# Optimization experiments

Hardware: AMD Instinct MI355X
Metric: run time of the kernel (lower is better)

The kernel has to match this reference:

```python
import jax, jax.numpy as jnp
import numpy as np

EPS_W = 1e-8   # weight reciprocal eps (matches torch code)
EPS_BN = 1e-5  # torch BatchNorm1d default eps


def _cdist(a, b):
    # a: [B,N,3], b: [B,M,3] -> [B,N,M] euclidean distances
    sq = (jnp.sum(a * a, -1)[:, :, None] + jnp.sum(b * b, -1)[:, None, :]
          - 2.0 * jnp.einsum('bnd,bmd->bnm', a, b))
    return jnp.sqrt(jnp.maximum(sq, 0.0))


def _bn_relu(x, gamma, beta):
    # x: [B,C,N]; training-mode batch norm over (B,N)
    mean = jnp.mean(x, axis=(0, 2), keepdims=True)
    var = jnp.mean((x - mean) ** 2, axis=(0, 2), keepdims=True)
    y = (x - mean) * jax.lax.rsqrt(var + EPS_BN)
    y = y * gamma[None, :, None] + beta[None, :, None]
    return jax.nn.relu(y)


def setup_inputs() -> dict:
    key = jax.random.key(0)
    ks = jax.random.split(key, 8)
    B, Np, Ns = 16, 1024, 4096
    Cp, Cs, Co = 256, 128, 256
    return {
        'xyz_prev': jax.random.normal(ks[0], (B, Np, 3), jnp.float32),
        'xyz_skip': jax.random.normal(ks[1], (B, Ns, 3), jnp.float32),
        'points_prev': jax.random.normal(ks[2], (B, Cp, Np), jnp.float32),
        'points_skip': jax.random.normal(ks[3], (B, Cs, Ns), jnp.float32),
        'W1': jax.random.normal(ks[4], (Co, Cp + Cs), jnp.float32) * 0.05,
        'g1': jnp.ones((Co,), jnp.float32),
        'b1': jnp.zeros((Co,), jnp.float32),
        'W2': jax.random.normal(ks[5], (Co, Co), jnp.float32) * 0.05,
        'g2': jnp.ones((Co,), jnp.float32),
        'b2': jnp.zeros((Co,), jnp.float32),
    }


def reference(xyz_prev, xyz_skip, points_prev, points_skip, W1, g1, b1, W2, g2, b2):
    dist = _cdist(xyz_skip, xyz_prev)                       # [B,Ns,Np]
    neg, idx = jax.lax.top_k(-dist, 3)                      # 3 smallest dists
    dist_recip = 1.0 / (dist + EPS_W)
    # NOTE: normalization is over ALL N_prev points (faithful to source)
    weight = dist_recip / jnp.sum(dist_recip, axis=2, keepdims=True)
    w3 = jnp.take_along_axis(weight, idx, axis=2)           # [B,Ns,3]
    pp = jnp.swapaxes(points_prev, 1, 2)                    # [B,Np,Cp]
    g = jnp.take_along_axis(pp[:, None, :, :], idx[..., None], axis=2)  # [B,Ns,3,Cp]
    interp = jnp.einsum('bnk,bnkc->bcn', w3, g)             # [B,Cp,Ns]
    x = jnp.concatenate([interp, points_skip], axis=1)      # [B,Cp+Cs,Ns]
    x = _bn_relu(jnp.einsum('bcn,oc->bon', x, W1), g1, b1)
    x = _bn_relu(jnp.einsum('bcn,oc->bon', x, W2), g2, b2)
    return x
```

## Files before the change

### kernel.cpp

```cpp
#include <hip/hip_runtime.h>
#include <math.h>

constexpr int NB  = 16;
constexpr int NP  = 1024;
constexpr int NS  = 4096;
constexpr int CP  = 256;
constexpr int CS  = 128;
constexpr int CIN = 384;
constexpr int CO  = 256;

constexpr int NCHUNK = 8;
constexpr int CHPTS  = NP / NCHUNK;

typedef unsigned int uint;
typedef unsigned short ushort_t;
typedef __attribute__((ext_vector_type(8))) short short8;
typedef __attribute__((ext_vector_type(4))) float f32x4;

__device__ __forceinline__ ushort_t f2bf(float f) {
  uint u = __float_as_uint(f);
  uint r = (u + 0x7fffu + ((u >> 16) & 1u)) >> 16;
  return (ushort_t)r;
}
__device__ __forceinline__ float bf2f(ushort_t u) {
  return __uint_as_float(((uint)u) << 16);
}

__device__ __forceinline__ void gload16(const void* g, void* l) {
  __builtin_amdgcn_global_load_lds(
      (const __attribute__((address_space(1))) uint*)g,
      (__attribute__((address_space(3))) uint*)l, 16, 0, 0);
}

__global__ __launch_bounds__(256) void topk_chunk_kernel(
    const float* __restrict__ xyz_prev, const float* __restrict__ xyz_skip,
    float* __restrict__ pbuf) {
  __shared__ float px[CHPTS], py[CHPTS], pz[CHPTS];
  int ng = blockIdx.x;
  int q  = blockIdx.y;
  int b  = blockIdx.z;
  int tid = threadIdx.x;
  if (tid < CHPTS) {
    const float* xp = xyz_prev + ((size_t)b * NP + q * CHPTS + tid) * 3;
    px[tid] = xp[0]; py[tid] = xp[1]; pz[tid] = xp[2];
  }
  __syncthreads();
  int n = ng * 256 + tid;
  const float* xq = xyz_skip + ((size_t)b * NS + n) * 3;
  float qx = xq[0], qy = xq[1], qz = xq[2];
  float d0 = INFINITY, d1 = INFINITY, d2 = INFINITY;
  int i0 = -1, i1 = -1, i2 = -1;
  float rsum = 0.f;
  int pbase = q * CHPTS;

  #define TK_BODY(PX, PY, PZ, PI)                                        \
    {                                                                    \
      float dx = (PX) - qx, dy = (PY) - qy, dz = (PZ) - qz;              \
      float sq = fmaf(dz, dz, fmaf(dy, dy, fmaf(dx, dx, 1e-16f)));       \
      rsum += __builtin_amdgcn_rsqf(sq);                                 \
      bool c0 = sq < d0, c1 = sq < d1, c2 = sq < d2;                     \
      int pi = (PI);                                                     \
      d2 = c2 ? (c1 ? d1 : sq) : d2;                                     \
      i2 = c2 ? (c1 ? i1 : pi) : i2;                                     \
      d1 = c1 ? (c0 ? d0 : sq) : d1;                                     \
      i1 = c1 ? (c0 ? i0 : pi) : i1;                                     \
      d0 = c0 ? sq : d0;                                                 \
      i0 = c0 ? pi : i0;                                                 \
    }

  for (int p = 0; p < CHPTS; p += 4) {
    float4 X = *(const float4*)&px[p];
    float4 Y = *(const float4*)&py[p];
    float4 Z = *(const float4*)&pz[p];
    TK_BODY(X.x, Y.x, Z.x, pbase + p + 0);
    TK_BODY(X.y, Y.y, Z.y, pbase + p + 1);
    TK_BODY(X.z, Y.z, Z.z, pbase + p + 2);
    TK_BODY(X.w, Y.w, Z.w, pbase + p + 3);
  }
  #undef TK_BODY

  size_t P = ((size_t)(b * NCHUNK + q) * NS + n) * 8;
  float4 v0 = make_float4(d0, d1, d2, rsum);
  float4 v1;
  v1.x = __int_as_float(i0); v1.y = __int_as_float(i1);
  v1.z = __int_as_float(i2); v1.w = 0.f;
  *(float4*)(pbuf + P) = v0;
  *(float4*)(pbuf + P + 4) = v1;
}

__global__ __launch_bounds__(256) void topk_merge_kernel(
    const float* __restrict__ pbuf, float* __restrict__ w3,
    int* __restrict__ idx3) {
  int gid = blockIdx.x * 256 + threadIdx.x;
  int b = gid >> 12;
  int n = gid & (NS - 1);
  float d0 = INFINITY, d1 = INFINITY, d2 = INFINITY;
  int i0 = -1, i1 = -1, i2 = -1;
  float rsum = 0.f;
  for (int q = 0; q < NCHUNK; q++) {
    size_t P = ((size_t)(b * NCHUNK + q) * NS + n) * 8;
    float4 v0 = *(const float4*)(pbuf + P);
    float4 v1 = *(const float4*)(pbuf + P + 4);
    rsum += v0.w;
    float ds[3] = {v0.x, v0.y, v0.z};
    int   is[3] = {__float_as_int(v1.x), __float_as_int(v1.y),
                   __float_as_int(v1.z)};
    #pragma unroll
    for (int k = 0; k < 3; k++) {
      float sq = ds[k]; int pi = is[k];
      bool c0 = sq < d0, c1 = sq < d1, c2 = sq < d2;
      d2 = c2 ? (c1 ? d1 : sq) : d2;
      i2 = c2 ? (c1 ? i1 : pi) : i2;
      d1 = c1 ? (c0 ? d0 : sq) : d1;
      i1 = c1 ? (c0 ? i0 : pi) : i1;
      d0 = c0 ? sq : d0;
      i0 = c0 ? pi : i0;
    }
  }
  float inv = 1.0f / rsum;
  size_t base = (size_t)gid * 3;
  w3[base + 0] = __builtin_amdgcn_rsqf(d0) * inv;
  w3[base + 1] = __builtin_amdgcn_rsqf(d1) * inv;
  w3[base + 2] = __builtin_amdgcn_rsqf(d2) * inv;
  idx3[base + 0] = i0; idx3[base + 1] = i1; idx3[base + 2] = i2;
}

__global__ __launch_bounds__(256) void wcast_kernel(
    const float* __restrict__ W1, const float* __restrict__ W2,
    ushort_t* __restrict__ W1b, ushort_t* __restrict__ W2b) {
  int t = blockIdx.x * 256 + threadIdx.x;
  int n1 = CO * CIN / 4;
  if (t < n1) {
    float4 v = *(const float4*)(W1 + t * 4);
    ushort4 o; o.x = f2bf(v.x); o.y = f2bf(v.y); o.z = f2bf(v.z); o.w = f2bf(v.w);
    *(ushort4*)(W1b + t * 4) = o;
  } else {
    int u = t - n1;
    float4 v = *(const float4*)(W2 + u * 4);
    ushort4 o; o.x = f2bf(v.x); o.y = f2bf(v.y); o.z = f2bf(v.z); o.w = f2bf(v.w);
    *(ushort4*)(W2b + u * 4) = o;
  }
}

__global__ __launch_bounds__(256) void ppT_kernel(
    const float* __restrict__ pp, ushort_t* __restrict__ pptT) {
  __shared__ float tl[64][65];
  int p0 = blockIdx.x * 64, c0 = blockIdx.y * 64, b = blockIdx.z;
  int tid = threadIdx.x;
  const float* P = pp + (size_t)b * CP * NP;
  int pi4 = (tid & 15) * 4, ci = tid >> 4;
  #pragma unroll
  for (int r = 0; r < 4; r++) {
    int cc = ci + 16 * r;
    float4 v = *(const float4*)(P + (size_t)(c0 + cc) * NP + p0 + pi4);
    tl[cc][pi4] = v.x; tl[cc][pi4 + 1] = v.y; tl[cc][pi4 + 2] = v.z; tl[cc][pi4 + 3] = v.w;
  }
  __syncthreads();
  ushort_t* O = pptT + (size_t)b * NP * CP;
  int ci4 = (tid & 15) * 4, pi = tid >> 4;
  #pragma unroll
  for (int r = 0; r < 4; r++) {
    int pr = pi + 16 * r;
    ushort4 o;
    o.x = f2bf(tl[ci4 + 0][pr]); o.y = f2bf(tl[ci4 + 1][pr]);
    o.z = f2bf(tl[ci4 + 2][pr]); o.w = f2bf(tl[ci4 + 3][pr]);
    *(ushort4*)(O + (size_t)(p0 + pr) * CP + c0 + ci4) = o;
  }
}

__global__ __launch_bounds__(256) void skipT_kernel(
    const float* __restrict__ sk, ushort_t* __restrict__ x1) {
  __shared__ float tl[64][65];
  int n0 = blockIdx.x * 64, c0 = blockIdx.y * 64, b = blockIdx.z;
  int tid = threadIdx.x;
  const float* S = sk + (size_t)b * CS * NS;
  int ni4 = (tid & 15) * 4, ci = tid >> 4;
  #pragma unroll
  for (int r = 0; r < 4; r++) {
    int cc = ci + 16 * r;
    float4 v = *(const float4*)(S + (size_t)(c0 + cc) * NS + n0 + ni4);
    tl[cc][ni4] = v.x; tl[cc][ni4 + 1] = v.y; tl[cc][ni4 + 2] = v.z; tl[cc][ni4 + 3] = v.w;
  }
  __syncthreads();
  ushort_t* O = x1 + (size_t)b * NS * CIN;
  int ci4 = (tid & 15) * 4, ni = tid >> 4;
  #pragma unroll
  for (int r = 0; r < 4; r++) {
    int nr = ni + 16 * r;
    ushort4 o;
    o.x = f2bf(tl[ci4 + 0][nr]); o.y = f2bf(tl[ci4 + 1][nr]);
    o.z = f2bf(tl[ci4 + 2][nr]); o.w = f2bf(tl[ci4 + 3][nr]);
    *(ushort4*)(O + (size_t)(n0 + nr) * CIN + CP + c0 + ci4) = o;
  }
}

__global__ __launch_bounds__(256) void interp_kernel(
    const ushort_t* __restrict__ pptT, const float* __restrict__ w3,
    const int* __restrict__ idx3, ushort_t* __restrict__ x1) {
  int tid = threadIdx.x;
  int nl = tid >> 6, l = tid & 63;
  int b = blockIdx.y;
  int n = blockIdx.x * 4 + nl;
  size_t nb = (size_t)b * NS + n;
  int j0 = idx3[nb * 3 + 0], j1 = idx3[nb * 3 + 1], j2 = idx3[nb * 3 + 2];
  float w0 = w3[nb * 3 + 0], w1 = w3[nb * 3 + 1], w2 = w3[nb * 3 + 2];
  const ushort_t* P = pptT + (size_t)b * NP * CP;
  int c = l * 4;
  ushort4 g0 = *(const ushort4*)(P + (size_t)j0 * CP + c);
  ushort4 g1 = *(const ushort4*)(P + (size_t)j1 * CP + c);
  ushort4 g2 = *(const ushort4*)(P + (size_t)j2 * CP + c);
  ushort4 o;
  o.x = f2bf(w0 * bf2f(g0.x) + w1 * bf2f(g1.x) + w2 * bf2f(g2.x));
  o.y = f2bf(w0 * bf2f(g0.y) + w1 * bf2f(g1.y) + w2 * bf2f(g2.y));
  o.z = f2bf(w0 * bf2f(g0.z) + w1 * bf2f(g1.z) + w2 * bf2f(g2.z));
  o.w = f2bf(w0 * bf2f(g0.w) + w1 * bf2f(g1.w) + w2 * bf2f(g2.w));
  *(ushort4*)(x1 + nb * CIN + c) = o;
}

template <int KD, bool OUT_BF16>
__global__ __launch_bounds__(256) void gemm_mfma_kernel(
    const ushort_t* __restrict__ X, const ushort_t* __restrict__ Wb,
    ushort_t* __restrict__ Yb, float* __restrict__ Yf,
    float* __restrict__ stats) {
  __shared__ ushort_t ldsX[128 * 32];
  __shared__ ushort_t ldsW[128 * 32];
  __shared__ float ssum[128], ssq[128];
  int tid = threadIdx.x;
  int w = tid >> 6, l = tid & 63;
  int n0 = blockIdx.x * 128;
  int by = blockIdx.y;
  int bz = blockIdx.z;
  if (tid < 128) { ssum[tid] = 0.f; ssq[tid] = 0.f; }

  f32x4 acc[4][4];
  #pragma unroll
  for (int i = 0; i < 4; i++)
    #pragma unroll
    for (int j = 0; j < 4; j++) acc[i][j] = {0.f, 0.f, 0.f, 0.f};

  int wn = (w & 1) * 64, wo = (w >> 1) * 64;
  int lr = l & 15, lk = l >> 4;
  const ushort_t* Xb = X + (size_t)bz * NS * KD;

  for (int kt = 0; kt < KD / 32; kt++) {
    int k0 = kt * 32;
    #pragma unroll
    for (int q = 0; q < 2; q++) {
      int r = q * 64 + w * 16 + (l >> 2);
      int cl = l & 3;
      int ks = k0 + 8 * (cl ^ ((r >> 1) & 3));
      gload16(Xb + (size_t)(n0 + r) * KD + ks, &ldsX[(q * 64 + w * 16) * 32]);
      gload16(Wb + (size_t)(by * 128 + r) * KD + ks, &ldsW[(q * 64 + w * 16) * 32]);
    }
    __syncthreads();
    short8 a[4], bfr[4];
    #pragma unroll
    for (int i = 0; i < 4; i++) {
      int rr = wn + i * 16 + lr;
      int cs = lk ^ ((rr >> 1) & 3);
      a[i] = *(const short8*)&ldsX[rr * 32 + cs * 8];
    }
    #pragma unroll
    for (int j = 0; j < 4; j++) {
      int rr = wo + j * 16 + lr;
      int cs = lk ^ ((rr >> 1) & 3);
      bfr[j] = *(const short8*)&ldsW[rr * 32 + cs * 8];
    }
    #pragma unroll
    for (int i = 0; i < 4; i++)
      #pragma unroll
      for (int j = 0; j < 4; j++)
        acc[i][j] = __builtin_amdgcn_mfma_f32_16x16x32_bf16(a[i], bfr[j], acc[i][j], 0, 0, 0);
    __syncthreads();
  }

  #pragma unroll
  for (int j = 0; j < 4; j++) {
    int ol = wo + j * 16 + lr;
    int og = by * 128 + ol;
    float ps = 0.f, pq = 0.f;
    #pragma unroll
    for (int i = 0; i < 4; i++) {
      #pragma unroll
      for (int rg = 0; rg < 4; rg++) {
        float v = acc[i][j][rg];
        ps += v; pq += v * v;
        int n = n0 + wn + i * 16 + lk * 4 + rg;
        size_t off = ((size_t)bz * NS + n) * CO + og;
        if (OUT_BF16) Yb[off] = f2bf(v);
        else Yf[off] = v;
      }
    }
    atomicAdd(&ssum[ol], ps);
    atomicAdd(&ssq[ol], pq);
  }
  __syncthreads();
  if (tid < 128) {
    atomicAdd(&stats[by * 128 + tid], ssum[tid]);
    atomicAdd(&stats[CO + by * 128 + tid], ssq[tid]);
  }
}

__global__ void bnstats_kernel(const float* __restrict__ stats,
                               const float* __restrict__ g,
                               const float* __restrict__ bt,
                               float* __restrict__ a, float* __restrict__ s) {
  int o = threadIdx.x;
  float cnt = (float)NB * (float)NS;
  float m = stats[o] / cnt;
  float var = stats[CO + o] / cnt - m * m;
  var = fmaxf(var, 0.f);
  float inv = rsqrtf(var + 1e-5f);
  float av = g[o] * inv;
  a[o] = av; s[o] = bt[o] - m * av;
}

__global__ __launch_bounds__(256) void act_kernel(
    ushort_t* __restrict__ y, const float* __restrict__ a,
    const float* __restrict__ s) {
  size_t i = ((size_t)blockIdx.x * 256 + threadIdx.x) * 8;
  int o = (int)(i & (CO - 1));
  ushort4 v0 = *(ushort4*)(y + i), v1 = *(ushort4*)(y + i + 4);
  ushort4 r0, r1;
  r0.x = f2bf(fmaxf(fmaf(a[o + 0], bf2f(v0.x), s[o + 0]), 0.f));
  r0.y = f2bf(fmaxf(fmaf(a[o + 1], bf2f(v0.y), s[o + 1]), 0.f));
  r0.z = f2bf(fmaxf(fmaf(a[o + 2], bf2f(v0.z), s[o + 2]), 0.f));
  r0.w = f2bf(fmaxf(fmaf(a[o + 3], bf2f(v0.w), s[o + 3]), 0.f));
  r1.x = f2bf(fmaxf(fmaf(a[o + 4], bf2f(v1.x), s[o + 4]), 0.f));
  r1.y = f2bf(fmaxf(fmaf(a[o + 5], bf2f(v1.y), s[o + 5]), 0.f));
  r1.z = f2bf(fmaxf(fmaf(a[o + 6], bf2f(v1.z), s[o + 6]), 0.f));
  r1.w = f2bf(fmaxf(fmaf(a[o + 7], bf2f(v1.w), s[o + 7]), 0.f));
  *(ushort4*)(y + i) = r0;
  *(ushort4*)(y + i + 4) = r1;
}

__global__ __launch_bounds__(256) void bnrelu_tr_kernel(
    const ushort_t* __restrict__ y2b, const float* __restrict__ a2,
    const float* __restrict__ s2, float* __restrict__ out) {
  __shared__ float tl[64][65];
  int n0 = blockIdx.x * 64, o0 = blockIdx.y * 64, b = blockIdx.z;
  const ushort_t* Y = y2b + (size_t)b * NS * CO;
  int tid = threadIdx.x;
  int o8 = (tid & 7) * 8, row = tid >> 3;
  #pragma unroll
  for (int r = 0; r < 2; r++) {
    int ii = row + 32 * r;
    const ushort_t* src = Y + (size_t)(n0 + ii) * CO + o0 + o8;
    ushort4 v0 = *(const ushort4*)(src);
    ushort4 v1 = *(const ushort4*)(src + 4);
    tl[ii][o8 + 0] = bf2f(v0.x); tl[ii][o8 + 1] = bf2f(v0.y);
    tl[ii][o8 + 2] = bf2f(v0.z); tl[ii][o8 + 3] = bf2f(v0.w);
    tl[ii][o8 + 4] = bf2f(v1.x); tl[ii][o8 + 5] = bf2f(v1.y);
    tl[ii][o8 + 6] = bf2f(v1.z); tl[ii][o8 + 7] = bf2f(v1.w);
  }
  __syncthreads();
  float* O = out + (size_t)b * CO * NS;
  int ii4 = (tid & 15) * 4, j = tid >> 4;
  #pragma unroll
  for (int r = 0; r < 4; r++) {
    int jj = j + 16 * r;
    float av = a2[o0 + jj], sv = s2[o0 + jj];
    float4 v;
    v.x = fmaxf(fmaf(av, tl[ii4 + 0][jj], sv), 0.f);
    v.y = fmaxf(fmaf(av, tl[ii4 + 1][jj], sv), 0.f);
    v.z = fmaxf(fmaf(av, tl[ii4 + 2][jj], sv), 0.f);
    v.w = fmaxf(fmaf(av, tl[ii4 + 3][jj], sv), 0.f);
    *(float4*)(O + (size_t)(o0 + jj) * NS + n0 + ii4) = v;
  }
}

__global__ void zero_kernel(float* st1, float* st2) {
  int t = threadIdx.x;
  if (t < 512) { st1[t] = 0.f; st2[t] = 0.f; }
}

extern "C" void kernel_launch(void* const* d_in, const int* in_sizes, int n_in,
                              void* d_out, int out_size, void* d_ws, size_t ws_size,
                              hipStream_t stream) {
  const float* xyz_prev    = (const float*)d_in[0];
  const float* xyz_skip    = (const float*)d_in[1];
  const float* points_prev = (const float*)d_in[2];
  const float* points_skip = (const float*)d_in[3];
  const float* W1 = (const float*)d_in[4];
  const float* g1 = (const float*)d_in[5];
  const float* b1 = (const float*)d_in[6];
  const float* W2 = (const float*)d_in[7];
  const float* g2 = (const float*)d_in[8];
  const float* b2 = (const float*)d_in[9];
  float* out = (float*)d_out;

  char* W = (char*)d_ws;
  size_t off = 0;
  auto alloc = [&](size_t bytes) {
    size_t o = off; off = (off + bytes + 255) & ~(size_t)255; return o;
  };
  ushort_t* x1   = (ushort_t*)(W + alloc((size_t)NB * NS * CIN * 2));
  ushort_t* y1b  = (ushort_t*)(W + alloc((size_t)NB * NS * CO * 2));
  ushort_t* pptT = (ushort_t*)(W + alloc((size_t)NB * NP * CP * 2));
  ushort_t* W1b  = (ushort_t*)(W + alloc((size_t)CO * CIN * 2));
  ushort_t* W2b  = (ushort_t*)(W + alloc((size_t)CO * CO * 2));
  float* w3   = (float*)(W + alloc((size_t)NB * NS * 3 * 4));
  int*   idx3 = (int*)(W + alloc((size_t)NB * NS * 3 * 4));
  float* st1  = (float*)(W + alloc(512 * 4));
  float* st2  = (float*)(W + alloc(512 * 4));
  float* ab   = (float*)(W + alloc(1024 * 4));
  float* a1 = ab, *s1 = ab + 256, *a2 = ab + 512, *s2 = ab + 768;
  size_t y2_off = alloc((size_t)NB * NS * CO * 2);
  bool full = (ws_size >= off);
  ushort_t* y2b = full ? (ushort_t*)(W + y2_off) : (ushort_t*)d_out;
  float* pbuf = full ? (float*)(W + y2_off) : (float*)d_out;

  hipLaunchKernelGGL(zero_kernel, dim3(1), dim3(512), 0, stream, st1, st2);
  hipLaunchKernelGGL(topk_chunk_kernel, dim3(NS / 256, NCHUNK, NB), dim3(256), 0,
                     stream, xyz_prev, xyz_skip, pbuf);
  hipLaunchKernelGGL(topk_merge_kernel, dim3(NB * NS / 256), dim3(256), 0, stream,
                     pbuf, w3, idx3);
  hipLaunchKernelGGL(wcast_kernel, dim3((CO * CIN / 4 + CO * CO / 4 + 255) / 256),
                     dim3(256), 0, stream, W1, W2, W1b, W2b);
  hipLaunchKernelGGL(ppT_kernel, dim3(NP / 64, CP / 64, NB), dim3(256), 0, stream,
                     points_prev, pptT);
  hipLaunchKernelGGL(skipT_kernel, dim3(NS / 64, CS / 64, NB), dim3(256), 0, stream,
                     points_skip, x1);
  hipLaunchKernelGGL(interp_kernel, dim3(NS / 4, NB), dim3(256), 0, stream,
                     pptT, w3, idx3, x1);
  hipLaunchKernelGGL((gemm_mfma_kernel<CIN, true>), dim3(NS / 128, 2, NB), dim3(256),
                     0, stream, x1, W1b, y1b, (float*)nullptr, st1);
  hipLaunchKernelGGL(bnstats_kernel, dim3(1), dim3(256), 0, stream, st1, g1, b1, a1, s1);
  hipLaunchKernelGGL(act_kernel, dim3((int)((size_t)NB * NS * CO / 8 / 256)),
                     dim3(256), 0, stream, y1b, a1, s1);
  hipLaunchKernelGGL((gemm_mfma_kernel<CO, true>), dim3(NS / 128, 2, NB), dim3(256),
                     0, stream, y1b, W2b, y2b, (float*)nullptr, st2);
  hipLaunchKernelGGL(bnstats_kernel, dim3(1), dim3(256), 0, stream, st2, g2, b2, a2, s2);
  if (full) {
    hipLaunchKernelGGL(bnrelu_tr_kernel, dim3(NS / 64, CO / 64, NB), dim3(256), 0,
                       stream, y2b, a2, s2, out);
  } else {
    float* stage = (float*)d_ws;
    hipLaunchKernelGGL(bnrelu_tr_kernel, dim3(NS / 64, CO / 64, NB), dim3(256), 0,
                       stream, y2b, a2, s2, stage);
    hipMemcpyAsync(out, stage, (size_t)NB * NS * CO * 4, hipMemcpyDeviceToDevice,
                   stream);
  }
}
```

Baseline: 190.0 us.

## Fuse BN1+ReLU into GEMM2 load, two queries per thread in top-k

The first-layer batch-norm+ReLU is now applied while staging X tiles for the second GEMM, which removes the separate act_kernel pass that read and wrote the full y1 tensor. Those tiles now go through registers instead of async global-to-LDS loads, which may hurt latency hiding. The top-k chunk kernel handles two query points per thread so each shared-memory point load is reused, and it uses med3/min for the sorted-distance updates. Zeroing of the stats buffers moves into the weight-cast kernel, which removes one launch.

Measured after the change: 176.7 us. 7.0% less time.

```diff
diff --git a/kernel.cpp b/kernel.cpp
--- a/kernel.cpp
+++ b/kernel.cpp
@@ -25,6 +25,9 @@
 __device__ __forceinline__ float bf2f(ushort_t u) {
   return __uint_as_float(((uint)u) << 16);
 }
+__device__ __forceinline__ uint pk2(ushort_t lo, ushort_t hi) {
+  return (uint)lo | ((uint)hi << 16);
+}
 
 __device__ __forceinline__ void gload16(const void* g, void* l) {
   __builtin_amdgcn_global_load_lds(
@@ -32,11 +35,26 @@
       (__attribute__((address_space(3))) uint*)l, 16, 0, 0);
 }
 
+__device__ __forceinline__ void tk_step(float pxv, float pyv, float pzv, int pi,
+                                        float qx, float qy, float qz,
+                                        float& d0, float& d1, float& d2,
+                                        int& i0, int& i1, int& i2, float& rsum) {
+  float dx = pxv - qx, dy = pyv - qy, dz = pzv - qz;
+  float sq = fmaf(dz, dz, fmaf(dy, dy, fmaf(dx, dx, 1e-16f)));
+  rsum += __builtin_amdgcn_rsqf(sq);
+  bool c0 = sq < d0, c1 = sq < d1, c2 = sq < d2;
+  i2 = c2 ? (c1 ? i1 : pi) : i2;
+  i1 = c1 ? (c0 ? i0 : pi) : i1;
+  i0 = c0 ? pi : i0;
+  d2 = __builtin_amdgcn_fmed3f(d1, d2, sq);
+  d1 = __builtin_amdgcn_fmed3f(d0, d1, sq);
+  d0 = fminf(d0, sq);
+}
+
 __global__ __launch_bounds__(256) void topk_chunk_kernel(
     const float* __restrict__ xyz_prev, const float* __restrict__ xyz_skip,
     float* __restrict__ pbuf) {
   __shared__ float px[CHPTS], py[CHPTS], pz[CHPTS];
-  int ng = blockIdx.x;
   int q  = blockIdx.y;
   int b  = blockIdx.z;
   int tid = threadIdx.x;
@@ -45,47 +63,44 @@
     px[tid] = xp[0]; py[tid] = xp[1]; pz[tid] = xp[2];
   }
   __syncthreads();
-  int n = ng * 256 + tid;
-  const float* xq = xyz_skip + ((size_t)b * NS + n) * 3;
-  float qx = xq[0], qy = xq[1], qz = xq[2];
-  float d0 = INFINITY, d1 = INFINITY, d2 = INFINITY;
-  int i0 = -1, i1 = -1, i2 = -1;
-  float rsum = 0.f;
+  int nA = blockIdx.x * 512 + tid;
+  int nB = nA + 256;
+  const float* xqA = xyz_skip + ((size_t)b * NS + nA) * 3;
+  const float* xqB = xyz_skip + ((size_t)b * NS + nB) * 3;
+  float qxA = xqA[0], qyA = xqA[1], qzA = xqA[2];
+  float qxB = xqB[0], qyB = xqB[1], qzB = xqB[2];
+  float dA0 = INFINITY, dA1 = INFINITY, dA2 = INFINITY;
+  float dB0 = INFINITY, dB1 = INFINITY, dB2 = INFINITY;
+  int iA0 = -1, iA1 = -1, iA2 = -1, iB0 = -1, iB1 = -1, iB2 = -1;
+  float rsA = 0.f, rsB = 0.f;
   int pbase = q * CHPTS;
-
-  #define TK_BODY(PX, PY, PZ, PI)                                        \
-    {                                                                    \
-      float dx = (PX) - qx, dy = (PY) - qy, dz = (PZ) - qz;              \
-      float sq = fmaf(dz, dz, fmaf(dy, dy, fmaf(dx, dx, 1e-16f)));       \
-      rsum += __builtin_amdgcn_rsqf(sq);                                 \
-      bool c0 = sq < d0, c1 = sq < d1, c2 = sq < d2;                     \
-      int pi = (PI);                                                     \
-      d2 = c2 ? (c1 ? d1 : sq) : d2;                                     \
-      i2 = c2 ? (c1 ? i1 : pi) : i2;                                     \
-      d1 = c1 ? (c0 ? d0 : sq) : d1;                                     \
-      i1 = c1 ? (c0 ? i0 : pi) : i1;                                     \
-      d0 = c0 ? sq : d0;                                                 \
-      i0 = c0 ? pi : i0;                                                 \
-    }
 
   for (int p = 0; p < CHPTS; p += 4) {
     float4 X = *(const float4*)&px[p];
     float4 Y = *(const float4*)&py[p];
     float4 Z = *(const float4*)&pz[p];
-    TK_BODY(X.x, Y.x, Z.x, pbase + p + 0);
-    TK_BODY(X.y, Y.y, Z.y, pbase + p + 1);
-    TK_BODY(X.z, Y.z, Z.z, pbase + p + 2);
-    TK_BODY(X.w, Y.w, Z.w, pbase + p + 3);
-  }
-  #undef TK_BODY
-
-  size_t P = ((size_t)(b * NCHUNK + q) * NS + n) * 8;
-  float4 v0 = make_float4(d0, d1, d2, rsum);
-  float4 v1;
-  v1.x = __int_as_float(i0); v1.y = __int_as_float(i1);
-  v1.z = __int_as_float(i2); v1.w = 0.f;
-  *(float4*)(pbuf + P) = v0;
-  *(float4*)(pbuf + P + 4) = v1;
+    tk_step(X.x, Y.x, Z.x, pbase + p + 0, qxA, qyA, qzA, dA0, dA1, dA2, iA0, iA1, iA2, rsA);
+    tk_step(X.x, Y.x, Z.x, pbase + p + 0, qxB, qyB, qzB, dB0, dB1, dB2, iB0, iB1, iB2, rsB);
+    tk_step(X.y, Y.y, Z.y, pbase + p + 1, qxA, qyA, qzA, dA0, dA1, dA2, iA0, iA1, iA2, rsA);
+    tk_step(X.y, Y.y, Z.y, pbase + p + 1, qxB, qyB, qzB, dB0, dB1, dB2, iB0, iB1, iB2, rsB);
+    tk_step(X.z, Y.z, Z.z, pbase + p + 2, qxA, qyA, qzA, dA0, dA1, dA2, iA0, iA1, iA2, rsA);
+    tk_step(X.z, Y.z, Z.z, pbase + p + 2, qxB, qyB, qzB, dB0, dB1, dB2, iB0, iB1, iB2, rsB);
+    tk_step(X.w, Y.w, Z.w, pbase + p + 3, qxA, qyA, qzA, dA0, dA1, dA2, iA0, iA1, iA2, rsA);
+    tk_step(X.w, Y.w, Z.w, pbase + p + 3, qxB, qyB, qzB, dB0, dB1, dB2, iB0, iB1, iB2, rsB);
+  }
+
+  size_t PA = ((size_t)(b * NCHUNK + q) * NS + nA) * 8;
+  size_t PB = ((size_t)(b * NCHUNK + q) * NS + nB) * 8;
+  float4 a0 = make_float4(dA0, dA1, dA2, rsA);
+  float4 a1; a1.x = __int_as_float(iA0); a1.y = __int_as_float(iA1);
+  a1.z = __int_as_float(iA2); a1.w = 0.f;
+  float4 b0 = make_float4(dB0, dB1, dB2, rsB);
+  float4 b1; b1.x = __int_as_float(iB0); b1.y = __int_as_float(iB1);
+  b1.z = __int_as_float(iB2); b1.w = 0.f;
+  *(float4*)(pbuf + PA) = a0;
+  *(float4*)(pbuf + PA + 4) = a1;
+  *(float4*)(pbuf + PB) = b0;
+  *(float4*)(pbuf + PB + 4) = b1;
 }
 
 __global__ __launch_bounds__(256) void topk_merge_kernel(
@@ -109,12 +124,12 @@
     for (int k = 0; k < 3; k++) {
       float sq = ds[k]; int pi = is[k];
       bool c0 = sq < d0, c1 = sq < d1, c2 = sq < d2;
-      d2 = c2 ? (c1 ? d1 : sq) : d2;
       i2 = c2 ? (c1 ? i1 : pi) : i2;
-      d1 = c1 ? (c0 ? d0 : sq) : d1;
       i1 = c1 ? (c0 ? i0 : pi) : i1;
-      d0 = c0 ? sq : d0;
       i0 = c0 ? pi : i0;
+      d2 = __builtin_amdgcn_fmed3f(d1, d2, sq);
+      d1 = __builtin_amdgcn_fmed3f(d0, d1, sq);
+      d0 = fminf(d0, sq);
     }
   }
   float inv = 1.0f / rsum;
@@ -127,8 +142,14 @@
 
 __global__ __launch_bounds__(256) void wcast_kernel(
     const float* __restrict__ W1, const float* __restrict__ W2,
-    ushort_t* __restrict__ W1b, ushort_t* __restrict__ W2b) {
-  int t = blockIdx.x * 256 + threadIdx.x;
+    ushort_t* __restrict__ W1b, ushort_t* __restrict__ W2b,
+    float* __restrict__ st1, float* __restrict__ st2) {
+  int tid = threadIdx.x;
+  if (blockIdx.x == 0) {
+    st1[tid] = 0.f; st1[tid + 256] = 0.f;
+    st2[tid] = 0.f; st2[tid + 256] = 0.f;
+  }
+  int t = blockIdx.x * 256 + tid;
   int n1 = CO * CIN / 4;
   if (t < n1) {
     float4 v = *(const float4*)(W1 + t * 4);
@@ -217,11 +238,11 @@
   *(ushort4*)(x1 + nb * CIN + c) = o;
 }
 
-template <int KD, bool OUT_BF16>
+template <int KD, bool ACT>
 __global__ __launch_bounds__(256) void gemm_mfma_kernel(
     const ushort_t* __restrict__ X, const ushort_t* __restrict__ Wb,
-    ushort_t* __restrict__ Yb, float* __restrict__ Yf,
-    float* __restrict__ stats) {
+    const float* __restrict__ aa, const float* __restrict__ ss,
+    ushort_t* __restrict__ Yb, float* __restrict__ stats) {
   __shared__ ushort_t ldsX[128 * 32];
   __shared__ ushort_t ldsW[128 * 32];
   __shared__ float ssum[128], ssq[128];
@@ -241,16 +262,46 @@
   int wn = (w & 1) * 64, wo = (w >> 1) * 64;
   int lr = l & 15, lk = l >> 4;
   const ushort_t* Xb = X + (size_t)bz * NS * KD;
+  int rbase = w * 16 + (l >> 2);
+  int cl = l & 3;
+  int ksw = 8 * (cl ^ ((rbase >> 1) & 3));
 
   for (int kt = 0; kt < KD / 32; kt++) {
     int k0 = kt * 32;
+    int ks = k0 + ksw;
     #pragma unroll
     for (int q = 0; q < 2; q++) {
-      int r = q * 64 + w * 16 + (l >> 2);
-      int cl = l & 3;
-      int ks = k0 + 8 * (cl ^ ((r >> 1) & 3));
-      gload16(Xb + (size_t)(n0 + r) * KD + ks, &ldsX[(q * 64 + w * 16) * 32]);
+      int r = q * 64 + rbase;
       gload16(Wb + (size_t)(by * 128 + r) * KD + ks, &ldsW[(q * 64 + w * 16) * 32]);
+    }
+    if constexpr (!ACT) {
+      #pragma unroll
+      for (int q = 0; q < 2; q++) {
+        int r = q * 64 + rbase;
+        gload16(Xb + (size_t)(n0 + r) * KD + ks, &ldsX[(q * 64 + w * 16) * 32]);
+      }
+    } else {
+      float4 av0 = *(const float4*)(aa + ks);
+      float4 av1 = *(const float4*)(aa + ks + 4);
+      float4 sv0 = *(const float4*)(ss + ks);
+      float4 sv1 = *(const float4*)(ss + ks + 4);
+      #pragma unroll
+      for (int q = 0; q < 2; q++) {
+        int r = q * 64 + rbase;
+        const ushort_t* src = Xb + (size_t)(n0 + r) * KD + ks;
+        ushort4 v0 = *(const ushort4*)(src);
+        ushort4 v1 = *(const ushort4*)(src + 4);
+        int4 o;
+        o.x = (int)pk2(f2bf(fmaxf(fmaf(av0.x, bf2f(v0.x), sv0.x), 0.f)),
+                       f2bf(fmaxf(fmaf(av0.y, bf2f(v0.y), sv0.y), 0.f)));
+        o.y = (int)pk2(f2bf(fmaxf(fmaf(av0.z, bf2f(v0.z), sv0.z), 0.f)),
+                       f2bf(fmaxf(fmaf(av0.w, bf2f(v0.w), sv0.w), 0.f)));
+        o.z = (int)pk2(f2bf(fmaxf(fmaf(av1.x, bf2f(v1.x), sv1.x), 0.f)),
+                       f2bf(fmaxf(fmaf(av1.y, bf2f(v1.y), sv1.y), 0.f)));
+        o.w = (int)pk2(f2bf(fmaxf(fmaf(av1.z, bf2f(v1.z), sv1.z), 0.f)),
+                       f2bf(fmaxf(fmaf(av1.w, bf2f(v1.w), sv1.w), 0.f)));
+        *(int4*)&ldsX[(q * 64 + w * 16) * 32 + l * 8] = o;
+      }
     }
     __syncthreads();
     short8 a[4], bfr[4];
@@ -286,9 +337,7 @@
         float v = acc[i][j][rg];
         ps += v; pq += v * v;
         int n = n0 + wn + i * 16 + lk * 4 + rg;
-        size_t off = ((size_t)bz * NS + n) * CO + og;
-        if (OUT_BF16) Yb[off] = f2bf(v);
-        else Yf[off] = v;
+        Yb[((size_t)bz * NS + n) * CO + og] = f2bf(v);
       }
     }
     atomicAdd(&ssum[ol], ps);
@@ -315,25 +364,6 @@
   a[o] = av; s[o] = bt[o] - m * av;
 }
 
-__global__ __launch_bounds__(256) void act_kernel(
-    ushort_t* __restrict__ y, const float* __restrict__ a,
-    const float* __restrict__ s) {
-  size_t i = ((size_t)blockIdx.x * 256 + threadIdx.x) * 8;
-  int o = (int)(i & (CO - 1));
-  ushort4 v0 = *(ushort4*)(y + i), v1 = *(ushort4*)(y + i + 4);
-  ushort4 r0, r1;
-  r0.x = f2bf(fmaxf(fmaf(a[o + 0], bf2f(v0.x), s[o + 0]), 0.f));
-  r0.y = f2bf(fmaxf(fmaf(a[o + 1], bf2f(v0.y), s[o + 1]), 0.f));
-  r0.z = f2bf(fmaxf(fmaf(a[o + 2], bf2f(v0.z), s[o + 2]), 0.f));
-  r0.w = f2bf(fmaxf(fmaf(a[o + 3], bf2f(v0.w), s[o + 3]), 0.f));
-  r1.x = f2bf(fmaxf(fmaf(a[o + 4], bf2f(v1.x), s[o + 4]), 0.f));
-  r1.y = f2bf(fmaxf(fmaf(a[o + 5], bf2f(v1.y), s[o + 5]), 0.f));
-  r1.z = f2bf(fmaxf(fmaf(a[o + 6], bf2f(v1.z), s[o + 6]), 0.f));
-  r1.w = f2bf(fmaxf(fmaf(a[o + 7], bf2f(v1.w), s[o + 7]), 0.f));
-  *(ushort4*)(y + i) = r0;
-  *(ushort4*)(y + i + 4) = r1;
-}
-
 __global__ __launch_bounds__(256) void bnrelu_tr_kernel(
     const ushort_t* __restrict__ y2b, const float* __restrict__ a2,
     const float* __restrict__ s2, float* __restrict__ out) {
@@ -367,11 +397,6 @@
     v.w = fmaxf(fmaf(av, tl[ii4 + 3][jj], sv), 0.f);
     *(float4*)(O + (size_t)(o0 + jj) * NS + n0 + ii4) = v;
   }
-}
-
-__global__ void zero_kernel(float* st1, float* st2) {
-  int t = threadIdx.x;
-  if (t < 512) { st1[t] = 0.f; st2[t] = 0.f; }
 }
 
 extern "C" void kernel_launch(void* const* d_in, const int* in_sizes, int n_in,
@@ -410,26 +435,24 @@
   ushort_t* y2b = full ? (ushort_t*)(W + y2_off) : (ushort_t*)d_out;
   float* pbuf = full ? (float*)(W + y2_off) : (float*)d_out;
 
-  hipLaunchKernelGGL(zero_kernel, dim3(1), dim3(512), 0, stream, st1, st2);
-  hipLaunchKernelGGL(topk_chunk_kernel, dim3(NS / 256, NCHUNK, NB), dim3(256), 0,
+  hipLaunchKernelGGL(topk_chunk_kernel, dim3(NS / 512, NCHUNK, NB), dim3(256), 0,
                      stream, xyz_prev, xyz_skip, pbuf);
   hipLaunchKernelGGL(topk_merge_kernel, dim3(NB * NS / 256), dim3(256), 0, stream,
                      pbuf, w3, idx3);
   hipLaunchKernelGGL(wcast_kernel, dim3((CO * CIN / 4 + CO * CO / 4 + 255) / 256),
-                     dim3(256), 0, stream, W1, W2, W1b, W2b);
+                     dim3(256), 0, stream, W1, W2, W1b, W2b, st1, st2);
   hipLaunchKernelGGL(ppT_kernel, dim3(NP / 64, CP / 64, NB), dim3(256), 0, stream,
                      points_prev, pptT);
   hipLaunchKernelGGL(skipT_kernel, dim3(NS / 64, CS / 64, NB), dim3(256), 0, stream,
                      points_skip, x1);
   hipLaunchKernelGGL(interp_kernel, dim3(NS / 4, NB), dim3(256), 0, stream,
                      pptT, w3, idx3, x1);
-  hipLaunchKernelGGL((gemm_mfma_kernel<CIN, true>), dim3(NS / 128, 2, NB), dim3(256),
-                     0, stream, x1, W1b, y1b, (float*)nullptr, st1);
+  hipLaunchKernelGGL((gemm_mfma_kernel<CIN, false>), dim3(NS / 128, 2, NB), dim3(256),
+                     0, stream, x1, W1b, (const float*)nullptr, (const float*)nullptr,
+                     y1b, st1);
   hipLaunchKernelGGL(bnstats_kernel, dim3(1), dim3(256), 0, stream, st1, g1, b1, a1, s1);
-  hipLaunchKernelGGL(act_kernel, dim3((int)((size_t)NB * NS * CO / 8 / 256)),
-                     dim3(256), 0, stream, y1b, a1, s1);
   hipLaunchKernelGGL((gemm_mfma_kernel<CO, true>), dim3(NS / 128, 2, NB), dim3(256),
-                     0, stream, y1b, W2b, y2b, (float*)nullptr, st2);
+                     0, stream, y1b, W2b, a1, s1, y2b, st2);
   hipLaunchKernelGGL(bnstats_kernel, dim3(1), dim3(256), 0, stream, st2, g2, b2, a2, s2);
   if (full) {
     hipLaunchKernelGGL(bnrelu_tr_kernel, dim3(NS / 64, CO / 64, NB), dim3(256), 0,
```
